# Kernel optimization log

Hardware: AMD Instinct MI355X
Metric: run time of the kernel (lower is better)

The kernel has to match this reference:

```python
import jax, jax.numpy as jnp
import numpy as np

C = 1.0          # curvature
ALPHA = 0.2      # LeakyReLU negative slope
MIN_NORM = 1e-15
MASK_VAL = -9e15

def artanh(x):
    x = jnp.clip(x, -1 + 1e-7, 1 - 1e-7)
    return 0.5 * (jnp.log1p(x) - jnp.log1p(-x))

def logmap0(x, c):
    sqrt_c = jnp.sqrt(c)
    norm = jnp.maximum(jnp.linalg.norm(x, axis=-1, keepdims=True), MIN_NORM)
    return x / (sqrt_c * norm) * artanh(sqrt_c * norm)

def expmap0(u, c):
    sqrt_c = jnp.sqrt(c)
    norm = jnp.maximum(jnp.linalg.norm(u, axis=-1, keepdims=True), MIN_NORM)
    return jnp.tanh(sqrt_c * norm) * u / (sqrt_c * norm)

def proj(x, c):
    norm = jnp.maximum(jnp.linalg.norm(x, axis=-1, keepdims=True), MIN_NORM)
    maxnorm = (1.0 - 1e-5) / jnp.sqrt(c)
    return jnp.where(norm > maxnorm, x / norm * maxnorm, x)

def setup_inputs() -> dict:
    key = jax.random.key(0)
    k1, k2, k3, k4, k5 = jax.random.split(key, 5)
    N, D, CLS = 8192, 128, 16
    # points on the Poincare ball (small norm, then projected)
    x = proj(jax.random.normal(k1, (N, D), jnp.float32) * 0.01, C)
    # sparse-ish adjacency, avg degree ~32, with self loops
    adj = jax.random.uniform(k2, (N, N)) < (32.0 / N)
    adj = adj | jnp.eye(N, dtype=bool)
    W = jax.random.normal(k3, (D, CLS), jnp.float32) * (1.0 / np.sqrt(D))
    b = jnp.zeros((CLS,), jnp.float32)
    a_src = jax.random.normal(k4, (CLS,), jnp.float32) * 0.1
    a_dst = jax.random.normal(k5, (CLS,), jnp.float32) * 0.1
    return {"x": x, "adj": adj, "W": W, "b": b, "a_src": a_src, "a_dst": a_dst}

def reference(x, adj, W, b, a_src, a_dst):
    # hyperbolic -> tangent space at origin, then linear map to n_classes
    h = logmap0(x, C) @ W + b                              # [N, CLS]
    # GAT scores: e_ij = LeakyReLU(a_src.h_i + a_dst.h_j)
    e = jax.nn.leaky_relu((h @ a_src)[:, None] + (h @ a_dst)[None, :], ALPHA)  # [N, N]
    e = jnp.where(adj, e, MASK_VAL)
    att = jax.nn.softmax(e, axis=-1)                       # row softmax over neighbors
    out = jax.nn.elu(att @ h)                              # aggregate + activation
    # back onto the manifold
    return proj(expmap0(out, C), C)
```

## Files before the change

### kernel.cpp

```cpp
#include <hip/hip_runtime.h>
#include <math.h>

#define NN   8192
#define DD   128
#define CLS  16
#define ALPHA 0.2f
#define SEGCAP 64

typedef unsigned int uv4 __attribute__((ext_vector_type(4)));

__global__ __launch_bounds__(256) void hat_feat(
    const float* __restrict__ x, const float* __restrict__ W,
    const float* __restrict__ b, const float* __restrict__ a_src,
    const float* __restrict__ a_dst, const unsigned char* __restrict__ adj,
    float* __restrict__ h, float* __restrict__ s, float* __restrict__ dv,
    int* __restrict__ flag)
{
    const int lane = threadIdx.x & 63;
    const int row  = (blockIdx.x << 2) + (threadIdx.x >> 6);

    if (blockIdx.x == 0 && threadIdx.x < 64) {
        const int i = threadIdx.x + 1;
        const int ok = ((i & 3) != 0) && (adj[(size_t)i * (NN + 1)] != 0);
        unsigned long long bb = __ballot(ok);
        if (threadIdx.x == 0) *flag = (__popcll(bb) > 24) ? 1 : 0;
    }

    const float* xr = x + (size_t)row * DD;
    float x0 = xr[lane];
    float x1 = xr[lane + 64];

    float nsq = x0 * x0 + x1 * x1;
    #pragma unroll
    for (int o = 32; o > 0; o >>= 1) nsq += __shfl_xor(nsq, o);

    float norm = fmaxf(sqrtf(nsq), 1e-15f);
    float t    = fminf(norm, 1.0f - 1e-7f);
    float art  = 0.5f * (log1pf(t) - log1pf(-t));
    float scl  = art / norm;
    x0 *= scl;
    x1 *= scl;

    float hc[CLS];
    #pragma unroll
    for (int c = 0; c < CLS; ++c)
        hc[c] = x0 * W[lane * CLS + c] + x1 * W[(lane + 64) * CLS + c];

    #pragma unroll
    for (int o = 32; o > 0; o >>= 1) {
        #pragma unroll
        for (int c = 0; c < CLS; ++c) hc[c] += __shfl_xor(hc[c], o);
    }

    float sv = 0.0f, dvv = 0.0f;
    #pragma unroll
    for (int c = 0; c < CLS; ++c) {
        hc[c] += b[c];
        sv  += hc[c] * a_src[c];
        dvv += hc[c] * a_dst[c];
    }

    if (lane == 0) {
        float* hr = h + (size_t)row * CLS;
        #pragma unroll
        for (int c = 0; c < CLS; ++c) hr[c] = hc[c];
        s[row]  = sv;
        dv[row] = dvv;
    }
}

__global__ __launch_bounds__(256) void hat_scan(
    const unsigned char* __restrict__ adj, const int* __restrict__ flag,
    int* __restrict__ nbr, int* __restrict__ cnt4)
{
    const int lane = threadIdx.x & 63;
    const int q    = threadIdx.x >> 6;
    const int row  = blockIdx.x;
    const bool bytemode = (*flag != 0);

    unsigned mask = 0u;
    if (bytemode) {
        const uv4* base = reinterpret_cast<const uv4*>(
            adj + (size_t)row * NN + q * 2048);
        const uv4 a = __builtin_nontemporal_load(base + lane);
        const uv4 c = __builtin_nontemporal_load(base + 64 + lane);
        #pragma unroll
        for (int d = 0; d < 4; ++d) {
            mask |= (((a[d] & 0x01010101u) * 0x01020408u) >> 28) << (d << 2);
            mask |= (((c[d] & 0x01010101u) * 0x01020408u) >> 28) << (16 + (d << 2));
        }
    } else {
        const uv4* base = reinterpret_cast<const uv4*>(
            reinterpret_cast<const unsigned int*>(adj) + (size_t)row * NN + q * 2048);
        #pragma unroll
        for (int it = 0; it < 4; ++it) {
            const uv4 A = __builtin_nontemporal_load(base + (it << 7) + lane);
            const uv4 B = __builtin_nontemporal_load(base + (it << 7) + 64 + lane);
            unsigned bits =  (unsigned)(A[0] != 0u)       | ((unsigned)(A[1] != 0u) << 1)
                          | ((unsigned)(A[2] != 0u) << 2) | ((unsigned)(A[3] != 0u) << 3)
                          | ((unsigned)(B[0] != 0u) << 4) | ((unsigned)(B[1] != 0u) << 5)
                          | ((unsigned)(B[2] != 0u) << 6) | ((unsigned)(B[3] != 0u) << 7);
            mask |= bits << (it << 3);
        }
    }

    const int c = __popc(mask);
    int off = c;
    #pragma unroll
    for (int o = 1; o < 64; o <<= 1) {
        int v = __shfl_up(off, o);
        if (lane >= o) off += v;
    }
    const int total = __shfl(off, 63);
    off -= c;

    int* sb = nbr + ((size_t)row * 4 + q) * SEGCAP;
    while (mask) {
        const int b = __builtin_ctz(mask);
        mask &= mask - 1;
        const int j = bytemode
            ? (q * 2048 + ((b >> 4) << 10) + (lane << 4) + (b & 15))
            : (q * 2048 + ((b >> 3) << 9) + (((b >> 2) & 1) << 8) + (lane << 2) + (b & 3));
        if (off < SEGCAP) sb[off] = j;
        ++off;
    }
    if (lane == 0) cnt4[row * 4 + q] = (total < SEGCAP) ? total : SEGCAP;
}

__global__ __launch_bounds__(256) void hat_agg(
    const float* __restrict__ h, const float* __restrict__ s,
    const float* __restrict__ dv, const int* __restrict__ nbr,
    const int* __restrict__ cnt4, float* __restrict__ out)
{
    const int lane = threadIdx.x & 63;
    const int row  = (blockIdx.x << 2) + (threadIdx.x >> 6);
    const int cc   = lane & 15;
    const int g    = lane >> 4;

    const float si = s[row];
    const int4 nq = *reinterpret_cast<const int4*>(cnt4 + row * 4);
    const int* rbase = nbr + (size_t)row * 4 * SEGCAP;

    float mx = -3.0e38f;
    #pragma unroll
    for (int q = 0; q < 4; ++q) {
        const int n = (&nq.x)[q];
        const int* sb = rbase + q * SEGCAP;
        for (int i = lane; i < n; i += 64) {
            float e = si + dv[sb[i]];
            e = (e > 0.0f) ? e : ALPHA * e;
            mx = fmaxf(mx, e);
        }
    }
    #pragma unroll
    for (int o = 32; o > 0; o >>= 1) mx = fmaxf(mx, __shfl_xor(mx, o));

    float l = 0.0f, acc = 0.0f;
    #pragma unroll
    for (int q = 0; q < 4; ++q) {
        const int n = (&nq.x)[q];
        const int* sb = rbase + q * SEGCAP;
        for (int base = 0; base < n; base += 4) {
            const int idx = base + g;
            if (idx < n) {
                const int j = sb[idx];
                float e = si + dv[j];
                e = (e > 0.0f) ? e : ALPHA * e;
                const float w = __expf(e - mx);
                l += w;
                acc = fmaf(w, h[(size_t)j * CLS + cc], acc);
            }
        }
    }
    l   += __shfl_xor(l, 16);   l   += __shfl_xor(l, 32);
    acc += __shfl_xor(acc, 16); acc += __shfl_xor(acc, 32);

    float* orow = out + (size_t)row * CLS;
    if (l > 0.0f) {
        float u = acc / l;
        u = (u > 0.0f) ? u : expm1f(u);
        float nsq = u * u;
        #pragma unroll
        for (int o = 8; o > 0; o >>= 1) nsq += __shfl_xor(nsq, o);
        float norm = fmaxf(sqrtf(nsq), 1e-15f);
        float th   = tanhf(norm);
        float sc2  = th / norm;
        const float maxnorm = 1.0f - 1e-5f;
        float sc3  = (th > maxnorm) ? (maxnorm / th) : 1.0f;
        if (lane < CLS) orow[lane] = u * sc2 * sc3;
    } else {
        if (lane < CLS) orow[lane] = 0.0f;
    }
}

extern "C" void kernel_launch(void* const* d_in, const int* in_sizes, int n_in,
                              void* d_out, int out_size, void* d_ws, size_t ws_size,
                              hipStream_t stream) {
    const float*         x     = (const float*)d_in[0];
    const unsigned char* adj   = (const unsigned char*)d_in[1];
    const float*         W     = (const float*)d_in[2];
    const float*         b     = (const float*)d_in[3];
    const float*         a_src = (const float*)d_in[4];
    const float*         a_dst = (const float*)d_in[5];
    float*               out   = (float*)d_out;

    float* h    = (float*)d_ws;
    float* s    = h + (size_t)NN * CLS;
    float* dv   = s + NN;
    int*   flag = (int*)(dv + NN);
    int*   cnt4 = flag + 1;
    int*   nbr  = cnt4 + (size_t)NN * 4;

    hat_feat<<<NN / 4, 256, 0, stream>>>(x, W, b, a_src, a_dst, adj, h, s, dv, flag);
    hat_scan<<<NN,     256, 0, stream>>>(adj, flag, nbr, cnt4);
    hat_agg <<<NN / 4, 256, 0, stream>>>(h, s, dv, nbr, cnt4, out);
}
```

Before: 72.04 us.

## Replace per-row wave scan with grid-stride adjacency scan using atomic neighbor append

The adjacency scan moves from one block per row, with ballot, prefix-sum and ordered segment writes, to a fixed grid of 2048 blocks that stream the matrix flat. Each nonzero is appended to its row's neighbor list through an atomicAdd on a per-row counter, which the feature kernel zeroes first. Aggregation now reads a single list of up to 256 entries per row instead of four segments of 64. The aim is to remove the per-row scan and launch overhead and to stream the adjacency with fewer, larger blocks. In exchange it adds atomic contention, gives a nondeterministic neighbor order (which changes float summation order), and drops the nontemporal loads.

```diff
diff --git a/kernel.cpp b/kernel.cpp
--- a/kernel.cpp
+++ b/kernel.cpp
@@ -5,7 +5,9 @@
 #define DD   128
 #define CLS  16
 #define ALPHA 0.2f
-#define SEGCAP 64
+#define CAP  256
+#define SCAN_BLOCKS 2048
+#define SCAN_THREADS (SCAN_BLOCKS * 256)
 
 typedef unsigned int uv4 __attribute__((ext_vector_type(4)));
 
@@ -14,10 +16,12 @@
     const float* __restrict__ b, const float* __restrict__ a_src,
     const float* __restrict__ a_dst, const unsigned char* __restrict__ adj,
     float* __restrict__ h, float* __restrict__ s, float* __restrict__ dv,
-    int* __restrict__ flag)
+    int* __restrict__ flag, int* __restrict__ cnt)
 {
     const int lane = threadIdx.x & 63;
     const int row  = (blockIdx.x << 2) + (threadIdx.x >> 6);
+
+    if (threadIdx.x < 4) cnt[(blockIdx.x << 2) + threadIdx.x] = 0;
 
     if (blockIdx.x == 0 && threadIdx.x < 64) {
         const int i = threadIdx.x + 1;
@@ -71,66 +75,56 @@
 
 __global__ __launch_bounds__(256) void hat_scan(
     const unsigned char* __restrict__ adj, const int* __restrict__ flag,
-    int* __restrict__ nbr, int* __restrict__ cnt4)
+    int* __restrict__ nbr, int* __restrict__ cnt)
 {
-    const int lane = threadIdx.x & 63;
-    const int q    = threadIdx.x >> 6;
-    const int row  = blockIdx.x;
-    const bool bytemode = (*flag != 0);
-
-    unsigned mask = 0u;
-    if (bytemode) {
-        const uv4* base = reinterpret_cast<const uv4*>(
-            adj + (size_t)row * NN + q * 2048);
-        const uv4 a = __builtin_nontemporal_load(base + lane);
-        const uv4 c = __builtin_nontemporal_load(base + 64 + lane);
-        #pragma unroll
-        for (int d = 0; d < 4; ++d) {
-            mask |= (((a[d] & 0x01010101u) * 0x01020408u) >> 28) << (d << 2);
-            mask |= (((c[d] & 0x01010101u) * 0x01020408u) >> 28) << (16 + (d << 2));
+    const int tid = blockIdx.x * 256 + threadIdx.x;
+    const uv4* base = reinterpret_cast<const uv4*>(adj);
+
+    if (*flag == 0) {
+        #pragma unroll 4
+        for (int k = 0; k < 32; ++k) {
+            const int u = k * SCAN_THREADS + tid;
+            const uv4 a = base[u];
+            if ((a[0] | a[1] | a[2] | a[3]) != 0u) {
+                const int row = u >> 11;
+                const int c0  = (u & 2047) << 2;
+                #pragma unroll
+                for (int d = 0; d < 4; ++d)
+                    if (a[d] != 0u) {
+                        const int pos = atomicAdd(&cnt[row], 1);
+                        if (pos < CAP) nbr[row * CAP + pos] = c0 + d;
+                    }
+            }
         }
     } else {
-        const uv4* base = reinterpret_cast<const uv4*>(
-            reinterpret_cast<const unsigned int*>(adj) + (size_t)row * NN + q * 2048);
-        #pragma unroll
-        for (int it = 0; it < 4; ++it) {
-            const uv4 A = __builtin_nontemporal_load(base + (it << 7) + lane);
-            const uv4 B = __builtin_nontemporal_load(base + (it << 7) + 64 + lane);
-            unsigned bits =  (unsigned)(A[0] != 0u)       | ((unsigned)(A[1] != 0u) << 1)
-                          | ((unsigned)(A[2] != 0u) << 2) | ((unsigned)(A[3] != 0u) << 3)
-                          | ((unsigned)(B[0] != 0u) << 4) | ((unsigned)(B[1] != 0u) << 5)
-                          | ((unsigned)(B[2] != 0u) << 6) | ((unsigned)(B[3] != 0u) << 7);
-            mask |= bits << (it << 3);
+        #pragma unroll 4
+        for (int k = 0; k < 8; ++k) {
+            const int u = k * SCAN_THREADS + tid;
+            const uv4 a = base[u];
+            if ((a[0] | a[1] | a[2] | a[3]) != 0u) {
+                const int row = u >> 9;
+                const int c0  = (u & 511) << 4;
+                #pragma unroll
+                for (int d = 0; d < 4; ++d) {
+                    const unsigned v = a[d];
+                    if (v != 0u) {
+                        #pragma unroll
+                        for (int bb = 0; bb < 4; ++bb)
+                            if ((v >> (bb * 8)) & 0xffu) {
+                                const int pos = atomicAdd(&cnt[row], 1);
+                                if (pos < CAP) nbr[row * CAP + pos] = c0 + (d << 2) + bb;
+                            }
+                    }
+                }
+            }
         }
     }
-
-    const int c = __popc(mask);
-    int off = c;
-    #pragma unroll
-    for (int o = 1; o < 64; o <<= 1) {
-        int v = __shfl_up(off, o);
-        if (lane >= o) off += v;
-    }
-    const int total = __shfl(off, 63);
-    off -= c;
-
-    int* sb = nbr + ((size_t)row * 4 + q) * SEGCAP;
-    while (mask) {
-        const int b = __builtin_ctz(mask);
-        mask &= mask - 1;
-        const int j = bytemode
-            ? (q * 2048 + ((b >> 4) << 10) + (lane << 4) + (b & 15))
-            : (q * 2048 + ((b >> 3) << 9) + (((b >> 2) & 1) << 8) + (lane << 2) + (b & 3));
-        if (off < SEGCAP) sb[off] = j;
-        ++off;
-    }
-    if (lane == 0) cnt4[row * 4 + q] = (total < SEGCAP) ? total : SEGCAP;
 }
 
 __global__ __launch_bounds__(256) void hat_agg(
     const float* __restrict__ h, const float* __restrict__ s,
     const float* __restrict__ dv, const int* __restrict__ nbr,
-    const int* __restrict__ cnt4, float* __restrict__ out)
+    const int* __restrict__ cnt, float* __restrict__ out)
 {
     const int lane = threadIdx.x & 63;
     const int row  = (blockIdx.x << 2) + (threadIdx.x >> 6);
@@ -138,38 +132,29 @@
     const int g    = lane >> 4;
 
     const float si = s[row];
-    const int4 nq = *reinterpret_cast<const int4*>(cnt4 + row * 4);
-    const int* rbase = nbr + (size_t)row * 4 * SEGCAP;
+    int n = cnt[row];
+    n = (n < CAP) ? n : CAP;
+    const int* rb = nbr + (size_t)row * CAP;
 
     float mx = -3.0e38f;
-    #pragma unroll
-    for (int q = 0; q < 4; ++q) {
-        const int n = (&nq.x)[q];
-        const int* sb = rbase + q * SEGCAP;
-        for (int i = lane; i < n; i += 64) {
-            float e = si + dv[sb[i]];
+    for (int i = lane; i < n; i += 64) {
+        float e = si + dv[rb[i]];
+        e = (e > 0.0f) ? e : ALPHA * e;
+        mx = fmaxf(mx, e);
+    }
+    #pragma unroll
+    for (int o = 32; o > 0; o >>= 1) mx = fmaxf(mx, __shfl_xor(mx, o));
+
+    float l = 0.0f, acc = 0.0f;
+    for (int base = 0; base < n; base += 4) {
+        const int idx = base + g;
+        if (idx < n) {
+            const int j = rb[idx];
+            float e = si + dv[j];
             e = (e > 0.0f) ? e : ALPHA * e;
-            mx = fmaxf(mx, e);
-        }
-    }
-    #pragma unroll
-    for (int o = 32; o > 0; o >>= 1) mx = fmaxf(mx, __shfl_xor(mx, o));
-
-    float l = 0.0f, acc = 0.0f;
-    #pragma unroll
-    for (int q = 0; q < 4; ++q) {
-        const int n = (&nq.x)[q];
-        const int* sb = rbase + q * SEGCAP;
-        for (int base = 0; base < n; base += 4) {
-            const int idx = base + g;
-            if (idx < n) {
-                const int j = sb[idx];
-                float e = si + dv[j];
-                e = (e > 0.0f) ? e : ALPHA * e;
-                const float w = __expf(e - mx);
-                l += w;
-                acc = fmaf(w, h[(size_t)j * CLS + cc], acc);
-            }
+            const float w = __expf(e - mx);
+            l += w;
+            acc = fmaf(w, h[(size_t)j * CLS + cc], acc);
         }
     }
     l   += __shfl_xor(l, 16);   l   += __shfl_xor(l, 32);
@@ -208,10 +193,11 @@
     float* s    = h + (size_t)NN * CLS;
     float* dv   = s + NN;
     int*   flag = (int*)(dv + NN);
-    int*   cnt4 = flag + 1;
-    int*   nbr  = cnt4 + (size_t)NN * 4;
-
-    hat_feat<<<NN / 4, 256, 0, stream>>>(x, W, b, a_src, a_dst, adj, h, s, dv, flag);
-    hat_scan<<<NN,     256, 0, stream>>>(adj, flag, nbr, cnt4);
-    hat_agg <<<NN / 4, 256, 0, stream>>>(h, s, dv, nbr, cnt4, out);
-}
+    int*   cnt  = flag + 1;
+    int*   nbr  = cnt + NN;
+
+    hat_feat<<<NN / 4,      256, 0, stream>>>(x, W, b, a_src, a_dst, adj,
+                                              h, s, dv, flag, cnt);
+    hat_scan<<<SCAN_BLOCKS, 256, 0, stream>>>(adj, flag, nbr, cnt);
+    hat_agg <<<NN / 4,      256, 0, stream>>>(h, s, dv, nbr, cnt, out);
+}
```

Result: slower. 91.82 us (+27.5%).
